# Optimization experiments

Measured on AMD Instinct MI355X. Metric: run time of the kernel, lower is better.

## Reference

```python
import jax, jax.numpy as jnp
import numpy as np

DIM = 256
HEADS = 4
HEAD_DIM = DIM // HEADS          # 64
KEY_DIM = HEAD_DIM // 2          # 32 (attn_ratio=0.5)
HIDDEN = DIM + 2 * KEY_DIM * HEADS  # 512
B, H, W = 2, 64, 64
EPS = 1e-5


def _conv2d(x, w, groups=1, pad=0):
    return jax.lax.conv_general_dilated(
        x, w, window_strides=(1, 1), padding=[(pad, pad), (pad, pad)],
        dimension_numbers=('NCHW', 'OIHW', 'NCHW'), feature_group_count=groups)


def _bn(x, g, b, m, v):
    scale = g / jnp.sqrt(v + EPS)
    return x * scale[None, :, None, None] + (b - m * scale)[None, :, None, None]


def setup_inputs() -> dict:
    key = jax.random.key(0)
    ks = jax.random.split(key, 16)
    d = {
        'x': jax.random.normal(ks[0], (B, DIM, H, W), jnp.float32),
        'qkv_w': jax.random.normal(ks[1], (HIDDEN, DIM, 1, 1), jnp.float32) * 0.05,
        'qkv_g': jax.random.uniform(ks[2], (HIDDEN,), jnp.float32, 0.5, 1.5),
        'qkv_b': jax.random.normal(ks[3], (HIDDEN,), jnp.float32) * 0.1,
        'qkv_m': jax.random.normal(ks[4], (HIDDEN,), jnp.float32) * 0.1,
        'qkv_v': jax.random.uniform(ks[5], (HIDDEN,), jnp.float32, 0.5, 1.5),
        'proj_w': jax.random.normal(ks[6], (DIM, DIM, 1, 1), jnp.float32) * 0.05,
        'proj_g': jax.random.uniform(ks[7], (DIM,), jnp.float32, 0.5, 1.5),
        'proj_b': jax.random.normal(ks[8], (DIM,), jnp.float32) * 0.1,
        'proj_m': jax.random.normal(ks[9], (DIM,), jnp.float32) * 0.1,
        'proj_v': jax.random.uniform(ks[10], (DIM,), jnp.float32, 0.5, 1.5),
        'pe_w': jax.random.normal(ks[11], (DIM, 1, 3, 3), jnp.float32) * 0.1,
        'pe_g': jax.random.uniform(ks[12], (DIM,), jnp.float32, 0.5, 1.5),
        'pe_b': jax.random.normal(ks[13], (DIM,), jnp.float32) * 0.1,
        'pe_m': jax.random.normal(ks[14], (DIM,), jnp.float32) * 0.1,
        'pe_v': jax.random.uniform(ks[15], (DIM,), jnp.float32, 0.5, 1.5),
    }
    return d


def reference(x, qkv_w, qkv_g, qkv_b, qkv_m, qkv_v,
              proj_w, proj_g, proj_b, proj_m, proj_v,
              pe_w, pe_g, pe_b, pe_m, pe_v):
    b, c, h, w = x.shape
    n = h * w
    scale = KEY_DIM ** -0.5

    qkv = _bn(_conv2d(x, qkv_w), qkv_g, qkv_b, qkv_m, qkv_v)  # [b, hidden, h, w]
    qkv = qkv.reshape(b, HEADS, 2 * KEY_DIM + HEAD_DIM, n)
    q = qkv[:, :, :KEY_DIM]                       # [b, heads, key_dim, n]
    k = qkv[:, :, KEY_DIM:2 * KEY_DIM]            # [b, heads, key_dim, n]
    v = qkv[:, :, 2 * KEY_DIM:]                   # [b, heads, head_dim, n]

    # attn[b,h,i,j] = sum_d q[b,h,d,i] * k[b,h,d,j] * scale; softmax over j
    attn = jnp.einsum('bhdi,bhdj->bhij', q, k) * scale
    attn = jax.nn.softmax(attn, axis=-1)

    # y = v @ attn^T : out[b,h,d,i] = sum_j v[b,h,d,j] * attn[b,h,i,j]
    y = jnp.einsum('bhdj,bhij->bhdi', v, attn).reshape(b, c, h, w)

    pe = _bn(_conv2d(v.reshape(b, c, h, w), pe_w, groups=c, pad=1),
             pe_g, pe_b, pe_m, pe_v)
    y = y + pe
    return _bn(_conv2d(y, proj_w), proj_g, proj_b, proj_m, proj_v)
```

## Files before the change

### kernel.cpp

```cpp
#include <hip/hip_runtime.h>
#include <hip/hip_bf16.h>

#define NSP 4096
#define BEPS 1e-5f
#define JSPLIT 4
#define JCHUNK (NSP / JSPLIT)

using short8  = __attribute__((ext_vector_type(8))) short;
using f32x4   = __attribute__((ext_vector_type(4))) float;

#define SCALE_LOG2E 0.25500526940103816f

__device__ __forceinline__ float b2f(unsigned short u) {
  return __uint_as_float(((unsigned)u) << 16);
}
__device__ __forceinline__ float b2f_lo(unsigned w) {
  return __uint_as_float(w << 16);
}
__device__ __forceinline__ float b2f_hi(unsigned w) {
  return __uint_as_float(w & 0xffff0000u);
}
__device__ __forceinline__ unsigned short f2b(float x) {
  unsigned u = __float_as_uint(x);
  u += 0x7fffu + ((u >> 16) & 1u);
  return (unsigned short)(u >> 16);
}
__device__ __forceinline__ unsigned pk_bf16(float a, float b) {
  return ((unsigned)f2b(b) << 16) | (unsigned)f2b(a);
}

__global__ __launch_bounds__(256) void cast_w_kernel(
    const float* __restrict__ qkv_w, const float* __restrict__ proj_w,
    unsigned short* __restrict__ wqb, unsigned short* __restrict__ wpb)
{
  const int i = blockIdx.x * 256 + threadIdx.x;
  if (i < 131072)       wqb[i] = f2b(qkv_w[i]);
  else                  wpb[i - 131072] = f2b(proj_w[i - 131072]);
}

__global__ __launch_bounds__(256) void transpose_x_kernel(
    const float* __restrict__ x, unsigned short* __restrict__ xT)
{
  const int n0 = blockIdx.x * 64, c0 = blockIdx.y * 64, b = blockIdx.z;
  __shared__ __align__(16) unsigned short tx[64][72];
  const int t = threadIdx.x;
  const int row = t >> 2;
  const int seg = t & 3;
  {
    const float* xp = x + ((size_t)(b * 256 + c0 + row)) * NSP + n0 + seg * 16;
    #pragma unroll
    for (int q4 = 0; q4 < 4; ++q4) {
      const float4 a = *reinterpret_cast<const float4*>(xp + q4 * 4);
      tx[seg * 16 + q4 * 4 + 0][row] = f2b(a.x);
      tx[seg * 16 + q4 * 4 + 1][row] = f2b(a.y);
      tx[seg * 16 + q4 * 4 + 2][row] = f2b(a.z);
      tx[seg * 16 + q4 * 4 + 3][row] = f2b(a.w);
    }
  }
  __syncthreads();
  const int nrow = t >> 2, ch = t & 3;
  unsigned short* op = xT + ((size_t)(b * NSP + n0 + nrow)) * 256 + c0 + ch * 16;
  *reinterpret_cast<float4*>(op)     = *reinterpret_cast<const float4*>(&tx[nrow][ch * 16]);
  *reinterpret_cast<float4*>(op + 8) = *reinterpret_cast<const float4*>(&tx[nrow][ch * 16 + 8]);
}

__global__ __launch_bounds__(256) void qkv_gemm_kernel(
    const unsigned short* __restrict__ xT, const unsigned short* __restrict__ wqb,
    const float* __restrict__ gg, const float* __restrict__ bb,
    const float* __restrict__ mm, const float* __restrict__ vv,
    unsigned short* __restrict__ qb, unsigned short* __restrict__ kb,
    unsigned short* __restrict__ vb)
{
  const int n0 = blockIdx.x * 128;
  const int cotile = blockIdx.y;
  const int b = blockIdx.z;
  const int co0 = cotile * 64;
  const int t = threadIdx.x;
  __shared__ __align__(16) unsigned short wt[64][136];
  __shared__ __align__(16) unsigned short xt[128][136];
  const int lane = t & 63, wave = t >> 6;
  const int m16 = lane & 15, quad = lane >> 4;

  f32x4 acc[8] = {};
  for (int kc = 0; kc < 2; ++kc) {
    if (kc) __syncthreads();
    {
      const unsigned short* wp = wqb + (size_t)(co0 + (t >> 2)) * 256 + kc * 128 + (t & 3) * 32;
      #pragma unroll
      for (int u = 0; u < 4; ++u)
        *reinterpret_cast<float4*>(&wt[t >> 2][(t & 3) * 32 + u * 8]) =
            *reinterpret_cast<const float4*>(wp + u * 8);
      const unsigned short* xp = xT + ((size_t)(b * NSP + n0 + (t >> 1))) * 256 + kc * 128 + (t & 1) * 64;
      #pragma unroll
      for (int u = 0; u < 8; ++u)
        *reinterpret_cast<float4*>(&xt[t >> 1][(t & 1) * 64 + u * 8]) =
            *reinterpret_cast<const float4*>(xp + u * 8);
    }
    __syncthreads();
    if ((cotile & 1) == 0) {
      #pragma unroll
      for (int ks = 0; ks < 4; ++ks) {
        const short8 af = *reinterpret_cast<const short8*>(&wt[wave * 16 + m16][ks * 32 + quad * 8]);
        #pragma unroll
        for (int nt = 0; nt < 8; ++nt) {
          const short8 bf = *reinterpret_cast<const short8*>(&xt[nt * 16 + m16][ks * 32 + quad * 8]);
          acc[nt] = __builtin_amdgcn_mfma_f32_16x16x32_bf16(af, bf, acc[nt], 0, 0, 0);
        }
      }
    } else {
      #pragma unroll
      for (int ks = 0; ks < 4; ++ks) {
        const short8 bf = *reinterpret_cast<const short8*>(&wt[wave * 16 + m16][ks * 32 + quad * 8]);
        #pragma unroll
        for (int nt = 0; nt < 8; ++nt) {
          const short8 af = *reinterpret_cast<const short8*>(&xt[nt * 16 + m16][ks * 32 + quad * 8]);
          acc[nt] = __builtin_amdgcn_mfma_f32_16x16x32_bf16(af, bf, acc[nt], 0, 0, 0);
        }
      }
    }
  }

  const int head = cotile >> 1;
  const int bh = b * 4 + head;
  if ((cotile & 1) == 0) {
    const int coh = wave * 16 + quad * 4;
    float sc[4], bi[4];
    #pragma unroll
    for (int r = 0; r < 4; ++r) {
      const int c = co0 + coh + r;
      sc[r] = gg[c] * rsqrtf(vv[c] + BEPS);
      bi[r] = bb[c] - mm[c] * sc[r];
    }
    unsigned short* dst = (coh < 32) ? qb : kb;
    const int d0 = coh & 31;
    #pragma unroll
    for (int nt = 0; nt < 8; ++nt) {
      const int i = n0 + nt * 16 + m16;
      uint2 pk2;
      pk2.x = pk_bf16(acc[nt][0] * sc[0] + bi[0], acc[nt][1] * sc[1] + bi[1]);
      pk2.y = pk_bf16(acc[nt][2] * sc[2] + bi[2], acc[nt][3] * sc[3] + bi[3]);
      *reinterpret_cast<uint2*>(dst + ((size_t)bh * NSP + i) * 32 + d0) = pk2;
    }
  } else {
    const int c = co0 + wave * 16 + m16;
    const float sc = gg[c] * rsqrtf(vv[c] + BEPS);
    const float bi = bb[c] - mm[c] * sc;
    const int d = wave * 16 + m16;
    #pragma unroll
    for (int nt = 0; nt < 8; ++nt) {
      const int j = n0 + nt * 16 + quad * 4;
      uint2 pk2;
      pk2.x = pk_bf16(acc[nt][0] * sc + bi, acc[nt][1] * sc + bi);
      pk2.y = pk_bf16(acc[nt][2] * sc + bi, acc[nt][3] * sc + bi);
      *reinterpret_cast<uint2*>(vb + ((size_t)(bh * 64 + d)) * NSP + j) = pk2;
    }
  }
}

__global__ __launch_bounds__(256, 4) void attn_kernel(
    const unsigned short* __restrict__ qb, const unsigned short* __restrict__ kb,
    const unsigned short* __restrict__ vb,
    unsigned short* __restrict__ Opart, float* __restrict__ lpart)
{
  const int i0    = blockIdx.x * 128;
  const int bh    = blockIdx.y;
  const int split = blockIdx.z;
  const int jbase = split * JCHUNK;
  const int t  = threadIdx.x;
  const int lane = t & 63, wave = t >> 6;
  const int m16 = lane & 15, quad = lane >> 4;
  __shared__ __align__(16) short smem[16384];
  short (*qs)[40] = (short(*)[40])smem;
  short (*ps)[72] = (short(*)[72])smem;
  short (*ks)[40] = (short(*)[40])(smem + 9216);
  short (*vs)[72] = (short(*)[72])(smem + 9216 + 2560);

  {
    const unsigned short* qp = qb + ((size_t)bh * NSP + i0) * 32;
    const int r = t >> 1, h = t & 1;
    *reinterpret_cast<float4*>(&qs[r][h * 16]) =
        *reinterpret_cast<const float4*>(qp + r * 32 + h * 16);
    *reinterpret_cast<float4*>(&qs[r][h * 16 + 8]) =
        *reinterpret_cast<const float4*>(qp + r * 32 + h * 16 + 8);
  }
  __syncthreads();
  short8 qfrag[2];
  qfrag[0] = *reinterpret_cast<const short8*>(&qs[wave * 32 + m16][quad * 8]);
  qfrag[1] = *reinterpret_cast<const short8*>(&qs[wave * 32 + 16 + m16][quad * 8]);

  float rsum[2] = {0.f, 0.f};
  f32x4 oacc[2][4] = {};

  const int srow = t >> 2, schunk = t & 3;
  for (int jt0 = 0; jt0 < JCHUNK; jt0 += 64) {
    const int j0 = jbase + jt0;
    __syncthreads();
    {
      const unsigned short* kp = kb + ((size_t)bh * NSP + j0) * 32;
      *reinterpret_cast<float4*>(&ks[srow][schunk * 8]) =
          *reinterpret_cast<const float4*>(kp + srow * 32 + schunk * 8);
      const unsigned short* vp = vb + (size_t)bh * 64 * NSP + j0;
      *reinterpret_cast<float4*>(&vs[srow][schunk * 16]) =
          *reinterpret_cast<const float4*>(vp + (size_t)srow * NSP + schunk * 16);
      *reinterpret_cast<float4*>(&vs[srow][schunk * 16 + 8]) =
          *reinterpret_cast<const float4*>(vp + (size_t)srow * NSP + schunk * 16 + 8);
    }
    __syncthreads();

    short8 kf[4];
    #pragma unroll
    for (int jt = 0; jt < 4; ++jt)
      kf[jt] = *reinterpret_cast<const short8*>(&ks[jt * 16 + m16][quad * 8]);

    #pragma unroll
    for (int it = 0; it < 2; ++it) {
      f32x4 sacc[4];
      #pragma unroll
      for (int jt = 0; jt < 4; ++jt)
        sacc[jt] = __builtin_amdgcn_mfma_f32_16x16x32_bf16(kf[jt], qfrag[it],
                                                           (f32x4){0.f,0.f,0.f,0.f}, 0, 0, 0);
      const int irow = wave * 32 + it * 16 + m16;
      #pragma unroll
      for (int jt = 0; jt < 4; ++jt) {
        float p0 = __builtin_amdgcn_exp2f(sacc[jt][0] * SCALE_LOG2E);
        float p1 = __builtin_amdgcn_exp2f(sacc[jt][1] * SCALE_LOG2E);
        float p2 = __builtin_amdgcn_exp2f(sacc[jt][2] * SCALE_LOG2E);
        float p3 = __builtin_amdgcn_exp2f(sacc[jt][3] * SCALE_LOG2E);
        rsum[it] += (p0 + p1) + (p2 + p3);
        uint2 pk2;
        pk2.x = pk_bf16(p0, p1);
        pk2.y = pk_bf16(p2, p3);
        *reinterpret_cast<uint2*>(&ps[irow][jt * 16 + quad * 4]) = pk2;
      }
    }

    short8 pa[2][2];
    #pragma unroll
    for (int it = 0; it < 2; ++it) {
      pa[it][0] = *reinterpret_cast<const short8*>(&ps[wave * 32 + it * 16 + m16][quad * 8]);
      pa[it][1] = *reinterpret_cast<const short8*>(&ps[wave * 32 + it * 16 + m16][32 + quad * 8]);
    }
    #pragma unroll
    for (int dt = 0; dt < 4; ++dt) {
      const short8 v0 = *reinterpret_cast<const short8*>(&vs[dt * 16 + m16][quad * 8]);
      const short8 v1 = *reinterpret_cast<const short8*>(&vs[dt * 16 + m16][32 + quad * 8]);
      #pragma unroll
      for (int it = 0; it < 2; ++it) {
        oacc[it][dt] = __builtin_amdgcn_mfma_f32_16x16x32_bf16(pa[it][0], v0, oacc[it][dt], 0, 0, 0);
        oacc[it][dt] = __builtin_amdgcn_mfma_f32_16x16x32_bf16(pa[it][1], v1, oacc[it][dt], 0, 0, 0);
      }
    }
  }

  #pragma unroll
  for (int it = 0; it < 2; ++it) {
    float rs = rsum[it];
    rs += __shfl_xor(rs, 16);
    rs += __shfl_xor(rs, 32);
    if (quad == 0)
      lpart[((size_t)split * 8 + bh) * NSP + i0 + wave * 32 + it * 16 + m16] = rs;
  }

  #pragma unroll
  for (int it = 0; it < 2; ++it)
    #pragma unroll
    for (int dt = 0; dt < 4; ++dt) {
      const int d = dt * 16 + m16;
      uint2 pk2;
      pk2.x = pk_bf16(oacc[it][dt][0], oacc[it][dt][1]);
      pk2.y = pk_bf16(oacc[it][dt][2], oacc[it][dt][3]);
      *reinterpret_cast<uint2*>(Opart +
          (((size_t)split * 8 + bh) * 64 + d) * NSP + i0 + wave * 32 + it * 16 + quad * 4) = pk2;
    }
}

__global__ __launch_bounds__(256) void fuse_kernel(
    const unsigned short* __restrict__ Opart, const float* __restrict__ lpart,
    const unsigned short* __restrict__ vb,
    const float* __restrict__ pw, const float* __restrict__ pg,
    const float* __restrict__ pb, const float* __restrict__ pm,
    const float* __restrict__ pv,
    unsigned short* __restrict__ yT)
{
  const int py = blockIdx.x;
  const int bh = blockIdx.y;
  const int b = bh >> 2, h = bh & 3;
  const int t = threadIdx.x;
  const int d = t >> 2, seg = t & 3;
  __shared__ float lsum[64];
  __shared__ __align__(16) unsigned short yt[64][72];

  if (t < 64) {
    float ls = 0.f;
    #pragma unroll
    for (int s = 0; s < JSPLIT; ++s)
      ls += lpart[((size_t)s * 8 + bh) * NSP + py * 64 + t];
    lsum[t] = ls;
  }
  __syncthreads();

  const int c = h * 64 + d;
  const int i0 = py * 64 + seg * 16;
  float os[16] = {};
  #pragma unroll
  for (int s = 0; s < JSPLIT; ++s) {
    const uint4* op = reinterpret_cast<const uint4*>(
        Opart + (((size_t)s * 8 + bh) * 64 + d) * NSP + i0);
    const uint4 a = op[0], e = op[1];
    os[0]  += b2f_lo(a.x); os[1]  += b2f_hi(a.x);
    os[2]  += b2f_lo(a.y); os[3]  += b2f_hi(a.y);
    os[4]  += b2f_lo(a.z); os[5]  += b2f_hi(a.z);
    os[6]  += b2f_lo(a.w); os[7]  += b2f_hi(a.w);
    os[8]  += b2f_lo(e.x); os[9]  += b2f_hi(e.x);
    os[10] += b2f_lo(e.y); os[11] += b2f_hi(e.y);
    os[12] += b2f_lo(e.z); os[13] += b2f_hi(e.z);
    os[14] += b2f_lo(e.w); os[15] += b2f_hi(e.w);
  }

  float w9[9];
  #pragma unroll
  for (int i = 0; i < 9; ++i) w9[i] = pw[c * 9 + i];
  const float sc = pg[c] * rsqrtf(pv[c] + BEPS);
  const float bi = pb[c] - pm[c] * sc;
  const unsigned short* vrow = vb + ((size_t)(bh * 64 + d)) * NSP;

  float conv[16] = {};
  #pragma unroll
  for (int dy = -1; dy <= 1; ++dy) {
    const int yy = py + dy;
    if (yy < 0 || yy > 63) continue;
    const unsigned short* vr = vrow + yy * 64 + seg * 16;
    float vals[18];
    const uint4 m0 = *reinterpret_cast<const uint4*>(vr);
    const uint4 m1 = *reinterpret_cast<const uint4*>(vr + 8);
    vals[1]  = b2f_lo(m0.x); vals[2]  = b2f_hi(m0.x);
    vals[3]  = b2f_lo(m0.y); vals[4]  = b2f_hi(m0.y);
    vals[5]  = b2f_lo(m0.z); vals[6]  = b2f_hi(m0.z);
    vals[7]  = b2f_lo(m0.w); vals[8]  = b2f_hi(m0.w);
    vals[9]  = b2f_lo(m1.x); vals[10] = b2f_hi(m1.x);
    vals[11] = b2f_lo(m1.y); vals[12] = b2f_hi(m1.y);
    vals[13] = b2f_lo(m1.z); vals[14] = b2f_hi(m1.z);
    vals[15] = b2f_lo(m1.w); vals[16] = b2f_hi(m1.w);
    vals[0]  = (seg > 0) ? b2f_hi(*reinterpret_cast<const unsigned*>(vr - 2)) : 0.f;
    vals[17] = (seg < 3) ? b2f_lo(*reinterpret_cast<const unsigned*>(vr + 16)) : 0.f;
    const float wr0 = w9[(dy + 1) * 3 + 0], wr1 = w9[(dy + 1) * 3 + 1], wr2 = w9[(dy + 1) * 3 + 2];
    #pragma unroll
    for (int u = 0; u < 16; ++u)
      conv[u] += vals[u] * wr0 + vals[u + 1] * wr1 + vals[u + 2] * wr2;
  }

  #pragma unroll
  for (int u = 0; u < 16; ++u) {
    const float yv = os[u] / lsum[seg * 16 + u] + conv[u] * sc + bi;
    yt[seg * 16 + u][d] = f2b(yv);
  }
  __syncthreads();

  const int prow = t >> 2, ch = t & 3;
  unsigned short* op = yT + ((size_t)(b * NSP + py * 64 + prow)) * 256 + h * 64 + ch * 16;
  *reinterpret_cast<float4*>(op)     = *reinterpret_cast<const float4*>(&yt[prow][ch * 16]);
  *reinterpret_cast<float4*>(op + 8) = *reinterpret_cast<const float4*>(&yt[prow][ch * 16 + 8]);
}

__global__ __launch_bounds__(256) void proj_gemm_kernel(
    const unsigned short* __restrict__ yT, const unsigned short* __restrict__ wpb,
    const float* __restrict__ gg, const float* __restrict__ bb,
    const float* __restrict__ mm, const float* __restrict__ vv,
    float* __restrict__ out)
{
  const int n0 = blockIdx.x * 128;
  const int co0 = blockIdx.y * 64;
  const int b = blockIdx.z;
  const int t = threadIdx.x;
  __shared__ __align__(16) unsigned short wt[64][136];
  __shared__ __align__(16) unsigned short yt[128][136];
  const int lane = t & 63, wave = t >> 6;
  const int m16 = lane & 15, quad = lane >> 4;

  f32x4 acc[8] = {};
  for (int kc = 0; kc < 2; ++kc) {
    if (kc) __syncthreads();
    {
      const unsigned short* wp = wpb + (size_t)(co0 + (t >> 2)) * 256 + kc * 128 + (t & 3) * 32;
      #pragma unroll
      for (int u = 0; u < 4; ++u)
        *reinterpret_cast<float4*>(&wt[t >> 2][(t & 3) * 32 + u * 8]) =
            *reinterpret_cast<const float4*>(wp + u * 8);
      const unsigned short* yp = yT + ((size_t)(b * NSP + n0 + (t >> 1))) * 256 + kc * 128 + (t & 1) * 64;
      #pragma unroll
      for (int u = 0; u < 8; ++u)
        *reinterpret_cast<float4*>(&yt[t >> 1][(t & 1) * 64 + u * 8]) =
            *reinterpret_cast<const float4*>(yp + u * 8);
    }
    __syncthreads();
    #pragma unroll
    for (int ks = 0; ks < 4; ++ks) {
      const short8 bf = *reinterpret_cast<const short8*>(&wt[wave * 16 + m16][ks * 32 + quad * 8]);
      #pragma unroll
      for (int nt = 0; nt < 8; ++nt) {
        const short8 af = *reinterpret_cast<const short8*>(&yt[nt * 16 + m16][ks * 32 + quad * 8]);
        acc[nt] = __builtin_amdgcn_mfma_f32_16x16x32_bf16(af, bf, acc[nt], 0, 0, 0);
      }
    }
  }

  const int c = co0 + wave * 16 + m16;
  const float sc = gg[c] * rsqrtf(vv[c] + BEPS);
  const float bi = bb[c] - mm[c] * sc;
  #pragma unroll
  for (int nt = 0; nt < 8; ++nt) {
    const int n = n0 + nt * 16 + quad * 4;
    float4 ov;
    ov.x = acc[nt][0] * sc + bi; ov.y = acc[nt][1] * sc + bi;
    ov.z = acc[nt][2] * sc + bi; ov.w = acc[nt][3] * sc + bi;
    *reinterpret_cast<float4*>(out + ((size_t)(b * 256 + c)) * NSP + n) = ov;
  }
}

extern "C" void kernel_launch(void* const* d_in, const int* in_sizes, int n_in,
                              void* d_out, int out_size, void* d_ws, size_t ws_size,
                              hipStream_t stream)
{
  const float* x      = (const float*)d_in[0];
  const float* qkv_w  = (const float*)d_in[1];
  const float* qkv_g  = (const float*)d_in[2];
  const float* qkv_b  = (const float*)d_in[3];
  const float* qkv_m  = (const float*)d_in[4];
  const float* qkv_v  = (const float*)d_in[5];
  const float* proj_w = (const float*)d_in[6];
  const float* proj_g = (const float*)d_in[7];
  const float* proj_b = (const float*)d_in[8];
  const float* proj_m = (const float*)d_in[9];
  const float* proj_v = (const float*)d_in[10];
  const float* pe_w   = (const float*)d_in[11];
  const float* pe_g   = (const float*)d_in[12];
  const float* pe_b   = (const float*)d_in[13];
  const float* pe_m   = (const float*)d_in[14];
  const float* pe_v   = (const float*)d_in[15];
  float* out = (float*)d_out;

  unsigned short* qb = (unsigned short*)d_ws;
  unsigned short* kb = qb + (size_t)8 * NSP * 32;
  unsigned short* vb = kb + (size_t)8 * NSP * 32;
  unsigned short* Opart = vb + (size_t)8 * 64 * NSP;
  float* lpart = (float*)(Opart + (size_t)JSPLIT * 8 * 64 * NSP);
  unsigned short* xT = (unsigned short*)(lpart + (size_t)JSPLIT * 8 * NSP);
  unsigned short* yT = xT + (size_t)2 * NSP * 256;
  unsigned short* wqb = yT + (size_t)2 * NSP * 256;
  unsigned short* wpb = wqb + (size_t)512 * 256;

  cast_w_kernel<<<dim3(768), 256, 0, stream>>>(qkv_w, proj_w, wqb, wpb);
  transpose_x_kernel<<<dim3(64, 4, 2), 256, 0, stream>>>(x, xT);
  qkv_gemm_kernel<<<dim3(32, 8, 2), 256, 0, stream>>>(xT, wqb, qkv_g, qkv_b, qkv_m, qkv_v,
                                                      qb, kb, vb);
  attn_kernel<<<dim3(32, 8, JSPLIT), 256, 0, stream>>>(qb, kb, vb, Opart, lpart);
  fuse_kernel<<<dim3(64, 8), 256, 0, stream>>>(Opart, lpart, vb,
                                               pe_w, pe_g, pe_b, pe_m, pe_v, yT);
  proj_gemm_kernel<<<dim3(32, 4, 2), 256, 0, stream>>>(yT, wpb, proj_g, proj_b, proj_m, proj_v,
                                                       out);
}
```

Before: 165.1 us.

## Fuse weight cast and input transpose into GEMM loads; halve proj GEMM tile

Removes the separate weight-cast and x-transpose kernels. The qkv GEMM now reads fp32 x and weights directly, converting to bf16 and transposing into shared memory as it loads. The proj GEMM casts its weights inline and uses 64-wide spatial tiles, doubling the grid so more blocks are in flight. This saves two launches and the round trip of the intermediate buffers, at the cost of redundant weight conversion per block and narrow strided shared-memory stores during the transpose.

Result: slower. 171.0 us (+3.5%).

```diff
diff --git a/kernel.cpp b/kernel.cpp
--- a/kernel.cpp
+++ b/kernel.cpp
@@ -29,43 +29,8 @@
   return ((unsigned)f2b(b) << 16) | (unsigned)f2b(a);
 }
 
-__global__ __launch_bounds__(256) void cast_w_kernel(
-    const float* __restrict__ qkv_w, const float* __restrict__ proj_w,
-    unsigned short* __restrict__ wqb, unsigned short* __restrict__ wpb)
-{
-  const int i = blockIdx.x * 256 + threadIdx.x;
-  if (i < 131072)       wqb[i] = f2b(qkv_w[i]);
-  else                  wpb[i - 131072] = f2b(proj_w[i - 131072]);
-}
-
-__global__ __launch_bounds__(256) void transpose_x_kernel(
-    const float* __restrict__ x, unsigned short* __restrict__ xT)
-{
-  const int n0 = blockIdx.x * 64, c0 = blockIdx.y * 64, b = blockIdx.z;
-  __shared__ __align__(16) unsigned short tx[64][72];
-  const int t = threadIdx.x;
-  const int row = t >> 2;
-  const int seg = t & 3;
-  {
-    const float* xp = x + ((size_t)(b * 256 + c0 + row)) * NSP + n0 + seg * 16;
-    #pragma unroll
-    for (int q4 = 0; q4 < 4; ++q4) {
-      const float4 a = *reinterpret_cast<const float4*>(xp + q4 * 4);
-      tx[seg * 16 + q4 * 4 + 0][row] = f2b(a.x);
-      tx[seg * 16 + q4 * 4 + 1][row] = f2b(a.y);
-      tx[seg * 16 + q4 * 4 + 2][row] = f2b(a.z);
-      tx[seg * 16 + q4 * 4 + 3][row] = f2b(a.w);
-    }
-  }
-  __syncthreads();
-  const int nrow = t >> 2, ch = t & 3;
-  unsigned short* op = xT + ((size_t)(b * NSP + n0 + nrow)) * 256 + c0 + ch * 16;
-  *reinterpret_cast<float4*>(op)     = *reinterpret_cast<const float4*>(&tx[nrow][ch * 16]);
-  *reinterpret_cast<float4*>(op + 8) = *reinterpret_cast<const float4*>(&tx[nrow][ch * 16 + 8]);
-}
-
 __global__ __launch_bounds__(256) void qkv_gemm_kernel(
-    const unsigned short* __restrict__ xT, const unsigned short* __restrict__ wqb,
+    const float* __restrict__ x, const float* __restrict__ qkv_w,
     const float* __restrict__ gg, const float* __restrict__ bb,
     const float* __restrict__ mm, const float* __restrict__ vv,
     unsigned short* __restrict__ qb, unsigned short* __restrict__ kb,
@@ -85,16 +50,27 @@
   for (int kc = 0; kc < 2; ++kc) {
     if (kc) __syncthreads();
     {
-      const unsigned short* wp = wqb + (size_t)(co0 + (t >> 2)) * 256 + kc * 128 + (t & 3) * 32;
-      #pragma unroll
-      for (int u = 0; u < 4; ++u)
-        *reinterpret_cast<float4*>(&wt[t >> 2][(t & 3) * 32 + u * 8]) =
-            *reinterpret_cast<const float4*>(wp + u * 8);
-      const unsigned short* xp = xT + ((size_t)(b * NSP + n0 + (t >> 1))) * 256 + kc * 128 + (t & 1) * 64;
-      #pragma unroll
-      for (int u = 0; u < 8; ++u)
-        *reinterpret_cast<float4*>(&xt[t >> 1][(t & 1) * 64 + u * 8]) =
-            *reinterpret_cast<const float4*>(xp + u * 8);
+      const int co = t >> 2, seg = t & 3;
+      const float* wp = qkv_w + (size_t)(co0 + co) * 256 + kc * 128 + seg * 32;
+      #pragma unroll
+      for (int u = 0; u < 8; ++u) {
+        const float4 a = *reinterpret_cast<const float4*>(wp + u * 4);
+        uint2 pk2; pk2.x = pk_bf16(a.x, a.y); pk2.y = pk_bf16(a.z, a.w);
+        *reinterpret_cast<uint2*>(&wt[co][seg * 32 + u * 4]) = pk2;
+      }
+      const int c2 = t >> 2, nseg = t & 3;
+      const float* xp0 = x + ((size_t)(b * 256 + kc * 128 + 2 * c2)) * NSP + n0 + nseg * 32;
+      const float* xp1 = xp0 + NSP;
+      #pragma unroll
+      for (int u4 = 0; u4 < 8; ++u4) {
+        const float4 r0 = *reinterpret_cast<const float4*>(xp0 + u4 * 4);
+        const float4 r1 = *reinterpret_cast<const float4*>(xp1 + u4 * 4);
+        const int nb = nseg * 32 + u4 * 4;
+        *reinterpret_cast<unsigned*>(&xt[nb + 0][2 * c2]) = pk_bf16(r0.x, r1.x);
+        *reinterpret_cast<unsigned*>(&xt[nb + 1][2 * c2]) = pk_bf16(r0.y, r1.y);
+        *reinterpret_cast<unsigned*>(&xt[nb + 2][2 * c2]) = pk_bf16(r0.z, r1.z);
+        *reinterpret_cast<unsigned*>(&xt[nb + 3][2 * c2]) = pk_bf16(r0.w, r1.w);
+      }
     }
     __syncthreads();
     if ((cotile & 1) == 0) {
@@ -363,33 +339,36 @@
 }
 
 __global__ __launch_bounds__(256) void proj_gemm_kernel(
-    const unsigned short* __restrict__ yT, const unsigned short* __restrict__ wpb,
+    const unsigned short* __restrict__ yT, const float* __restrict__ proj_w,
     const float* __restrict__ gg, const float* __restrict__ bb,
     const float* __restrict__ mm, const float* __restrict__ vv,
     float* __restrict__ out)
 {
-  const int n0 = blockIdx.x * 128;
+  const int n0 = blockIdx.x * 64;
   const int co0 = blockIdx.y * 64;
   const int b = blockIdx.z;
   const int t = threadIdx.x;
   __shared__ __align__(16) unsigned short wt[64][136];
-  __shared__ __align__(16) unsigned short yt[128][136];
+  __shared__ __align__(16) unsigned short yt[64][136];
   const int lane = t & 63, wave = t >> 6;
   const int m16 = lane & 15, quad = lane >> 4;
-
-  f32x4 acc[8] = {};
+  const int row = t >> 2, seg = t & 3;
+
+  f32x4 acc[4] = {};
   for (int kc = 0; kc < 2; ++kc) {
     if (kc) __syncthreads();
     {
-      const unsigned short* wp = wpb + (size_t)(co0 + (t >> 2)) * 256 + kc * 128 + (t & 3) * 32;
+      const float* wp = proj_w + (size_t)(co0 + row) * 256 + kc * 128 + seg * 32;
+      #pragma unroll
+      for (int u = 0; u < 8; ++u) {
+        const float4 a = *reinterpret_cast<const float4*>(wp + u * 4);
+        uint2 pk2; pk2.x = pk_bf16(a.x, a.y); pk2.y = pk_bf16(a.z, a.w);
+        *reinterpret_cast<uint2*>(&wt[row][seg * 32 + u * 4]) = pk2;
+      }
+      const unsigned short* yp = yT + ((size_t)(b * NSP + n0 + row)) * 256 + kc * 128 + seg * 32;
       #pragma unroll
       for (int u = 0; u < 4; ++u)
-        *reinterpret_cast<float4*>(&wt[t >> 2][(t & 3) * 32 + u * 8]) =
-            *reinterpret_cast<const float4*>(wp + u * 8);
-      const unsigned short* yp = yT + ((size_t)(b * NSP + n0 + (t >> 1))) * 256 + kc * 128 + (t & 1) * 64;
-      #pragma unroll
-      for (int u = 0; u < 8; ++u)
-        *reinterpret_cast<float4*>(&yt[t >> 1][(t & 1) * 64 + u * 8]) =
+        *reinterpret_cast<float4*>(&yt[row][seg * 32 + u * 8]) =
             *reinterpret_cast<const float4*>(yp + u * 8);
     }
     __syncthreads();
@@ -397,7 +376,7 @@
     for (int ks = 0; ks < 4; ++ks) {
       const short8 bf = *reinterpret_cast<const short8*>(&wt[wave * 16 + m16][ks * 32 + quad * 8]);
       #pragma unroll
-      for (int nt = 0; nt < 8; ++nt) {
+      for (int nt = 0; nt < 4; ++nt) {
         const short8 af = *reinterpret_cast<const short8*>(&yt[nt * 16 + m16][ks * 32 + quad * 8]);
         acc[nt] = __builtin_amdgcn_mfma_f32_16x16x32_bf16(af, bf, acc[nt], 0, 0, 0);
       }
@@ -408,7 +387,7 @@
   const float sc = gg[c] * rsqrtf(vv[c] + BEPS);
   const float bi = bb[c] - mm[c] * sc;
   #pragma unroll
-  for (int nt = 0; nt < 8; ++nt) {
+  for (int nt = 0; nt < 4; ++nt) {
     const int n = n0 + nt * 16 + quad * 4;
     float4 ov;
     ov.x = acc[nt][0] * sc + bi; ov.y = acc[nt][1] * sc + bi;
@@ -444,18 +423,13 @@
   unsigned short* vb = kb + (size_t)8 * NSP * 32;
   unsigned short* Opart = vb + (size_t)8 * 64 * NSP;
   float* lpart = (float*)(Opart + (size_t)JSPLIT * 8 * 64 * NSP);
-  unsigned short* xT = (unsigned short*)(lpart + (size_t)JSPLIT * 8 * NSP);
-  unsigned short* yT = xT + (size_t)2 * NSP * 256;
-  unsigned short* wqb = yT + (size_t)2 * NSP * 256;
-  unsigned short* wpb = wqb + (size_t)512 * 256;
-
-  cast_w_kernel<<<dim3(768), 256, 0, stream>>>(qkv_w, proj_w, wqb, wpb);
-  transpose_x_kernel<<<dim3(64, 4, 2), 256, 0, stream>>>(x, xT);
-  qkv_gemm_kernel<<<dim3(32, 8, 2), 256, 0, stream>>>(xT, wqb, qkv_g, qkv_b, qkv_m, qkv_v,
+  unsigned short* yT = (unsigned short*)(lpart + (size_t)JSPLIT * 8 * NSP);
+
+  qkv_gemm_kernel<<<dim3(32, 8, 2), 256, 0, stream>>>(x, qkv_w, qkv_g, qkv_b, qkv_m, qkv_v,
                                                       qb, kb, vb);
   attn_kernel<<<dim3(32, 8, JSPLIT), 256, 0, stream>>>(qb, kb, vb, Opart, lpart);
   fuse_kernel<<<dim3(64, 8), 256, 0, stream>>>(Opart, lpart, vb,
                                                pe_w, pe_g, pe_b, pe_m, pe_v, yT);
-  proj_gemm_kernel<<<dim3(32, 4, 2), 256, 0, stream>>>(yT, wpb, proj_g, proj_b, proj_m, proj_v,
+  proj_gemm_kernel<<<dim3(64, 4, 2), 256, 0, stream>>>(yT, proj_w, proj_g, proj_b, proj_m, proj_v,
                                                        out);
 }
```
